# Optimization experiments

Measured on AMD Instinct MI355X. Metric: run time of the kernel, lower is better.

## Reference

```python
import jax, jax.numpy as jnp
import numpy as np

EMBED_DIM = 1024
N_HEADS = 16
KV_SIZE = 64
CLIP_DIST = 10
SLEN = 1024
BSZ = 8


def setup_inputs() -> dict:
    key = jax.random.key(0)
    ks = jax.random.split(key, 7)
    s = 0.02
    inputs = jax.random.normal(ks[0], (SLEN, BSZ, EMBED_DIM), dtype=jnp.float32)
    W_in = jax.random.normal(ks[1], (3 * N_HEADS * KV_SIZE, EMBED_DIM), dtype=jnp.float32) * s
    b_in = jnp.zeros((3 * N_HEADS * KV_SIZE,), dtype=jnp.float32)
    k_dist_emb = jax.random.normal(ks[2], (CLIP_DIST + 1, KV_SIZE), dtype=jnp.float32) * s
    v_dist_emb = jax.random.normal(ks[3], (CLIP_DIST + 1, KV_SIZE), dtype=jnp.float32) * s
    W_out = jax.random.normal(ks[4], (EMBED_DIM, N_HEADS * KV_SIZE), dtype=jnp.float32) * s
    b_out = jnp.zeros((EMBED_DIM,), dtype=jnp.float32)
    return {"inputs": inputs, "W_in": W_in, "b_in": b_in,
            "k_dist_emb": k_dist_emb, "v_dist_emb": v_dist_emb,
            "W_out": W_out, "b_out": b_out}


def reference(inputs, W_in, b_in, k_dist_emb, v_dist_emb, W_out, b_out):
    slen, bsz, _ = inputs.shape
    h, d = N_HEADS, KV_SIZE
    # in_proj: (slen, bsz, 3*h*d) -> (3, bsz, h, slen, d)
    qkv = inputs @ W_in.T + b_in
    qkv = qkv.reshape(slen, bsz, 3, h, d).transpose(2, 1, 3, 0, 4)
    q, k, v = qkv[0], qkv[1], qkv[2]
    q = q * (d ** -0.5)
    # clipped absolute relative distances (slen, slen)
    idx = jnp.arange(slen)
    dist = jnp.minimum(jnp.abs(idx[None, :] - idx[:, None]), CLIP_DIST)
    k_dist = k_dist_emb[dist]  # (slen, slen, d)
    v_dist = v_dist_emb[dist]  # (slen, slen, d)
    # content scores + relative-distance bias
    attn = jnp.einsum('bhsd,bhtd->bhst', q, k) + jnp.einsum('bhsd,std->bhst', q, k_dist)
    attn = jax.nn.softmax(attn, axis=-1)
    # value accumulation + relative-distance value correction
    out = jnp.einsum('bhst,bhtd->bhsd', attn, v) + jnp.einsum('bhst,std->bhsd', attn, v_dist)
    # (bsz, h, slen, d) -> (slen, bsz, h*d)
    out = out.transpose(2, 0, 1, 3).reshape(slen, bsz, h * d)
    return out @ W_out.T + b_out
```

## Files before the change

### kernel.cpp

```cpp
#include <hip/hip_runtime.h>
#include <hip/hip_bf16.h>
#include <cstdint>


typedef __attribute__((ext_vector_type(8))) __bf16 bf16x8;
typedef __attribute__((ext_vector_type(4))) __bf16 bf16x4;
typedef __attribute__((ext_vector_type(4))) short s16x4;
typedef __attribute__((ext_vector_type(4))) float f32x4;

#if __has_builtin(__builtin_amdgcn_exp2f)
#define EXP2F(x) __builtin_amdgcn_exp2f(x)
#else
#define EXP2F(x) exp2f(x)
#endif

#if __has_builtin(__builtin_amdgcn_mfma_f32_16x16x16bf16_1k)
#define PV_MFMA(ACC, AV, BV) \
  ACC = __builtin_amdgcn_mfma_f32_16x16x16bf16_1k( \
      __builtin_bit_cast(s16x4, AV), __builtin_bit_cast(s16x4, BV), ACC, 0, 0, 0)
#elif __has_builtin(__builtin_amdgcn_mfma_f32_16x16x16_bf16)
#define PV_MFMA(ACC, AV, BV) \
  ACC = __builtin_amdgcn_mfma_f32_16x16x16_bf16(AV, BV, ACC, 0, 0, 0)
#else
#define PV_MFMA(ACC, AV, BV)                                               \
  asm volatile("s_nop 1\n\tv_mfma_f32_16x16x16_bf16 %0, %1, %2, %0\n\t"    \
               "s_nop 7\n\ts_nop 7"                                        \
               : "+v"(ACC)                                                 \
               : "v"(__builtin_bit_cast(s16x4, AV)),                       \
                 "v"(__builtin_bit_cast(s16x4, BV)))
#endif

__device__ __forceinline__ void gload_lds16(const void* g, void* l) {
  __builtin_amdgcn_global_load_lds(
      (const __attribute__((address_space(1))) void*)g,
      (__attribute__((address_space(3))) void*)l, 16, 0, 0);
}

__global__ __launch_bounds__(256) void f2b3_kernel(
    const float* __restrict__ s0, __bf16* __restrict__ d0,
    const float* __restrict__ s1, __bf16* __restrict__ d1,
    const float* __restrict__ s2, __bf16* __restrict__ d2) {
  int i = (blockIdx.x * 256 + threadIdx.x) * 8;
  const float* s; __bf16* d; int off;
  if (i < 8388608) { s = s0; d = d0; off = i; }
  else if (i < 11534336) { s = s1; d = d1; off = i - 8388608; }
  else { s = s2; d = d2; off = i - 11534336; }
  float4 a = *(const float4*)(s + off);
  float4 b = *(const float4*)(s + off + 4);
  bf16x8 o;
  o[0] = (__bf16)a.x; o[1] = (__bf16)a.y; o[2] = (__bf16)a.z; o[3] = (__bf16)a.w;
  o[4] = (__bf16)b.x; o[5] = (__bf16)b.y; o[6] = (__bf16)b.z; o[7] = (__bf16)b.w;
  *(bf16x8*)(d + off) = o;
}


#define STG8A(SL, TK, G)                                                      \
  gload_lds16(A + (size_t)(m0 + (G) * 64 + (tid >> 3)) * K + (TK) * 64 + sgc, \
              (void*)&sG[SL][(G) * 4096 + wave * 512]);
#define STG8B(SL, TK, G)                                                      \
  gload_lds16(Bp + (size_t)(n0 + (G) * 64 + (tid >> 3)) * K + (TK) * 64 + sgc,\
              (void*)&sG[SL][16384 + (G) * 4096 + wave * 512]);

#define GPH(SL, MP, NP, STAGE_STMT, TAIL_STMT)                                  \
  {                                                                             \
    bf16x8 af[2][2], bfr[2][2];                                                 \
    _Pragma("unroll") for (int mi = 0; mi < 2; ++mi)                            \
      _Pragma("unroll") for (int kk = 0; kk < 2; ++kk)                          \
        af[mi][kk] = *(const bf16x8*)&sG[SL][                                   \
            (wr * 64 + ((MP) * 2 + mi) * 16 + lr) * 64 +                        \
            (((kk * 4 + lg) ^ (lr & 7)) * 8)];                                  \
    _Pragma("unroll") for (int ni = 0; ni < 2; ++ni)                            \
      _Pragma("unroll") for (int kk = 0; kk < 2; ++kk)                          \
        bfr[ni][kk] = *(const bf16x8*)&sG[SL][16384 +                           \
            (wc * 64 + ((NP) * 2 + ni) * 16 + lr) * 64 +                        \
            (((kk * 4 + lg) ^ (lr & 7)) * 8)];                                  \
    STAGE_STMT                                                                  \
    __builtin_amdgcn_s_barrier();                                               \
    asm volatile("s_waitcnt lgkmcnt(0)" ::: "memory");                          \
    __builtin_amdgcn_sched_barrier(0);                                          \
    __builtin_amdgcn_s_setprio(1);                                              \
    _Pragma("unroll") for (int mi = 0; mi < 2; ++mi)                            \
      _Pragma("unroll") for (int ni = 0; ni < 2; ++ni)                          \
        _Pragma("unroll") for (int kk = 0; kk < 2; ++kk)                        \
          acc[(MP) * 2 + mi][(NP) * 2 + ni] =                                   \
              __builtin_amdgcn_mfma_f32_16x16x32_bf16(                          \
                  af[mi][kk], bfr[ni][kk],                                      \
                  acc[(MP) * 2 + mi][(NP) * 2 + ni], 0, 0, 0);                  \
    __builtin_amdgcn_s_setprio(0);                                              \
    TAIL_STMT                                                                   \
    __builtin_amdgcn_s_barrier();                                               \
  }

#define GTILE(SL, SS, TK2, DOSTG, WAITC)                                        \
  GPH(SL, 0, 0, if (DOSTG) { STG8A(SS, TK2, 0) STG8A(SS, TK2, 1) }, )           \
  GPH(SL, 0, 1, if (DOSTG) { STG8A(SS, TK2, 2) STG8A(SS, TK2, 3) }, )           \
  GPH(SL, 1, 0, if (DOSTG) { STG8B(SS, TK2, 0) }, )                             \
  GPH(SL, 1, 1, if (DOSTG) { STG8B(SS, TK2, 1) },                               \
      if ((WAITC) == 6) { asm volatile("s_waitcnt vmcnt(6)" ::: "memory"); }    \
      else if ((WAITC) == 0) { asm volatile("s_waitcnt vmcnt(0)" ::: "memory"); })

template <int EPI>
__global__ __launch_bounds__(512) void gemm8p(
    const __bf16* __restrict__ A, const __bf16* __restrict__ Bp,
    const float* __restrict__ bias, int K,
    float* __restrict__ outF, __bf16* __restrict__ outT, int N, int NT, int CPX) {
  __shared__ __align__(16) __bf16 sG[3][24576];
  const int tid = threadIdx.x;
  const int wave = tid >> 6, lane = tid & 63;
  const int lg = lane >> 4, lr = lane & 15;
  const int wr = wave >> 1, wc = wave & 1;
  const int lid = (blockIdx.x & 7) * CPX + (blockIdx.x >> 3);
  const int m0 = (lid / NT) * 256;
  const int n0 = (lid % NT) * 128;

  const int sgc = ((tid & 7) ^ ((tid >> 3) & 7)) * 8;

  f32x4 acc[4][4] = {};

  STG8A(0, 0, 0) STG8A(0, 0, 1) STG8A(0, 0, 2) STG8A(0, 0, 3)
  STG8B(0, 0, 0) STG8B(0, 0, 1)
  STG8A(1, 1, 0) STG8A(1, 1, 1) STG8A(1, 1, 2) STG8A(1, 1, 3)
  STG8B(1, 1, 0) STG8B(1, 1, 1)
  asm volatile("s_waitcnt vmcnt(6)" ::: "memory");
  __builtin_amdgcn_s_barrier();

  GTILE(0, 2, 2, 1, 6)
  GTILE(1, 0, 3, 1, 6)
  GTILE(2, 1, 4, 1, 6)
  GTILE(0, 2, 5, 1, 6)
  GTILE(1, 0, 6, 1, 6)
  GTILE(2, 1, 7, 1, 6)
  GTILE(0, 2, 8, 1, 6)
  GTILE(1, 0, 9, 1, 6)
  GTILE(2, 1, 10, 1, 6)
  GTILE(0, 2, 11, 1, 6)
  GTILE(1, 0, 12, 1, 6)
  GTILE(2, 1, 13, 1, 6)
  GTILE(0, 2, 14, 1, 6)
  GTILE(1, 0, 15, 1, 6)
  GTILE(2, 1, 16, 0, 0)
  GTILE(0, 2, 17, 0, 2)

#pragma unroll
  for (int mf = 0; mf < 4; ++mf) {
    const int gm0 = m0 + wr * 64 + mf * 16 + lg * 4;
#pragma unroll
    for (int nf = 0; nf < 4; ++nf) {
      const int gn = n0 + wc * 64 + nf * 16 + lr;
      const float bv = bias[gn];
#pragma unroll
      for (int rg = 0; rg < 4; ++rg) {
        const int gm = gm0 + rg;
        float v = acc[mf][nf][rg] + bv;
        if constexpr (EPI == 0) {
          int t = gn >> 10, h = (gn >> 6) & 15, d = gn & 63;
          int s = gm >> 3, b = gm & 7;
          if (t == 0) v *= 0.18033688011112042f;
          outT[(((size_t)((t * 8 + b) * 16 + h) * 1024 + s) << 6) + d] = (__bf16)v;
        } else {
          outF[(size_t)gm * N + gn] = v;
        }
      }
    }
  }
}

__global__ __launch_bounds__(256) void vtrans_kernel(const __bf16* __restrict__ v,
                                                     __bf16* __restrict__ vt) {
  __shared__ __bf16 tile[64][66];
  const int tid = threadIdx.x;
  const int bh = blockIdx.x >> 4;
  const int s0 = (blockIdx.x & 15) * 64;
  const __bf16* src = v + ((size_t)bh * 1024 + s0) * 64;
#pragma unroll
  for (int it = 0; it < 4; ++it) {
    int idx = it * 256 + tid;
    int r = idx >> 4, c4 = (idx & 15) * 4;
    bf16x4 x = *(const bf16x4*)&src[r * 64 + c4];
    tile[r][c4 + 0] = x[0]; tile[r][c4 + 1] = x[1];
    tile[r][c4 + 2] = x[2]; tile[r][c4 + 3] = x[3];
  }
  __syncthreads();
  __bf16* dst = vt + (size_t)bh * 65536;
#pragma unroll
  for (int it = 0; it < 4; ++it) {
    int idx = it * 256 + tid;
    int dr = idx >> 4, s4 = (idx & 15) * 4;
    bf16x4 y;
    y[0] = tile[s4 + 0][dr]; y[1] = tile[s4 + 1][dr];
    y[2] = tile[s4 + 2][dr]; y[3] = tile[s4 + 3][dr];
    *(bf16x4*)&dst[(size_t)dr * 1024 + s0 + s4] = y;
  }
}

#define ATTN_TILE(KT, KC, KS, VC, VS)                                           \
  {                                                                             \
    if ((KT) < 15)                                                              \
      gload_lds16(vtp + (size_t)srow * 1024 + ((KT) + 1) * 64 + sc8,            \
                  &sV[VS][wave * 512]);                                         \
    if ((KT) < 14)                                                              \
      gload_lds16(kp + (size_t)((KT) * 64 + 128 + srow) * 64 + sc8,             \
                  &sK[KS][wave * 512]);                                         \
    f32x4 sf[4];                                                                \
    __builtin_amdgcn_s_setprio(1);                                              \
    _Pragma("unroll") for (int tj = 0; tj < 4; ++tj) {                          \
      const int t = tj * 16 + lr;                                               \
      bf16x8 bk0 = *(const bf16x8*)&sK[KC][t * 64 + ((lg ^ (t & 7)) * 8)];      \
      bf16x8 bk1 = *(const bf16x8*)&sK[KC][t * 64 + (((4 + lg) ^ (t & 7)) * 8)];\
      f32x4 z = {};                                                             \
      z = __builtin_amdgcn_mfma_f32_16x16x32_bf16(bk0, aq[0], z, 0, 0, 0);      \
      z = __builtin_amdgcn_mfma_f32_16x16x32_bf16(bk1, aq[1], z, 0, 0, 0);      \
      sf[tj] = z;                                                               \
    }                                                                           \
    __builtin_amdgcn_s_setprio(0);                                              \
    const bool inband = ((KT) * 64 <= sb + 24) && ((KT) * 64 + 63 >= sb - 9);   \
    if (inband) {                                                               \
      const float* bDrow = &sBD[wave][lr][0];                                   \
      _Pragma("unroll") for (int tj = 0; tj < 4; ++tj) {                        \
        _Pragma("unroll") for (int rg = 0; rg < 4; ++rg) {                      \
          const int t = (KT) * 64 + tj * 16 + lg * 4 + rg;                      \
          const int dd = t - s;                                                 \
          const int ad = dd < 0 ? -dd : dd;                                     \
          if (ad <= 9) {                                                        \
            const float val = sf[tj][rg] + bDrow[ad];                           \
            sf[tj][rg] = val;                                                   \
            band[wave][lr][dd + 9] = (__bf16)val;                               \
          }                                                                     \
        }                                                                       \
      }                                                                         \
    }                                                                           \
    float vm[4];                                                                \
    _Pragma("unroll") for (int tj = 0; tj < 4; ++tj)                            \
      vm[tj] = fmaxf(fmaxf(sf[tj][0], sf[tj][1]), fmaxf(sf[tj][2], sf[tj][3])); \
    float vmax = fmaxf(fmaxf(vm[0], vm[1]), fmaxf(vm[2], vm[3]));               \
    vmax = fmaxf(vmax, __shfl_xor(vmax, 16, 64));                               \
    vmax = fmaxf(vmax, __shfl_xor(vmax, 32, 64));                               \
    if (__any(vmax > m + 8.f)) {                                                \
      const float mn = fmaxf(m, vmax);                                          \
      const float scl = EXP2F(m - mn);                                          \
      m = mn;                                                                   \
      l *= scl;                                                                 \
      _Pragma("unroll") for (int dj = 0; dj < 4; ++dj)                          \
        _Pragma("unroll") for (int rg = 0; rg < 4; ++rg)                        \
          o_acc[dj][rg] *= scl;                                                 \
    }                                                                           \
    float rs[4];                                                                \
    _Pragma("unroll") for (int tj = 0; tj < 4; ++tj) {                          \
      float p0 = EXP2F(sf[tj][0] - m), p1 = EXP2F(sf[tj][1] - m);               \
      float p2 = EXP2F(sf[tj][2] - m), p3 = EXP2F(sf[tj][3] - m);               \
      sf[tj][0] = p0; sf[tj][1] = p1; sf[tj][2] = p2; sf[tj][3] = p3;           \
      rs[tj] = (p0 + p1) + (p2 + p3);                                           \
    }                                                                           \
    float rsum = (rs[0] + rs[1]) + (rs[2] + rs[3]);                             \
    rsum += __shfl_xor(rsum, 16, 64);                                           \
    rsum += __shfl_xor(rsum, 32, 64);                                           \
    l += rsum;                                                                  \
    bf16x4 pbv[4];                                                              \
    _Pragma("unroll") for (int tj = 0; tj < 4; ++tj) {                          \
      pbv[tj][0] = (__bf16)sf[tj][0]; pbv[tj][1] = (__bf16)sf[tj][1];           \
      pbv[tj][2] = (__bf16)sf[tj][2]; pbv[tj][3] = (__bf16)sf[tj][3];           \
    }                                                                           \
    __builtin_amdgcn_s_setprio(1);                                              \
    _Pragma("unroll") for (int tj = 0; tj < 4; ++tj) {                          \
      _Pragma("unroll") for (int dj = 0; dj < 4; ++dj) {                        \
        const int d = dj * 16 + lr;                                             \
        const int ch = (2 * tj + (lg >> 1)) ^ (d & 7);                          \
        const bf16x4 av = *(const bf16x4*)&sV[VC][d * 64 + ch * 8 + (lg & 1) * 4]; \
        PV_MFMA(o_acc[dj], av, pbv[tj]);                                        \
      }                                                                         \
    }                                                                           \
    __builtin_amdgcn_s_setprio(0);                                              \
    if ((KT) < 14) {                                                            \
      asm volatile("s_waitcnt vmcnt(1)" ::: "memory");                          \
    } else if ((KT) == 14) {                                                    \
      asm volatile("s_waitcnt vmcnt(0)" ::: "memory");                          \
    }                                                                           \
    if ((KT) < 15) __builtin_amdgcn_s_barrier();                                \
  }

__global__ __launch_bounds__(512) void attn_kernel(
    const __bf16* __restrict__ qkv, const __bf16* __restrict__ vt,
    const float* __restrict__ kde, const float* __restrict__ vde,
    __bf16* __restrict__ O) {
  __shared__ __align__(16) __bf16 sK[3][4096];
  __shared__ __align__(16) __bf16 sV[2][4096];
  __shared__ __bf16 band[8][16][20];
  __shared__ float sBD[8][16][10];
  const int tid = threadIdx.x, wave = tid >> 6, lane = tid & 63;
  const int lg = lane >> 4, lr = lane & 15;
  const int lid = (blockIdx.x & 7) * 128 + (blockIdx.x >> 3);
  const int bh = lid >> 3;
  const int stile = lid & 7;
  const int sb = stile * 128 + wave * 16;
  const int b = bh >> 4, h = bh & 15;
  const __bf16* qp = qkv + (size_t)bh * 65536;
  const __bf16* kp = qkv + (size_t)(128 + bh) * 65536;
  const __bf16* vtp = vt + (size_t)bh * 65536;

  const int srow = tid >> 3;
  const int sc8 = ((tid & 7) ^ (srow & 7)) * 8;

  gload_lds16(kp + (size_t)srow * 64 + sc8, &sK[0][wave * 512]);
  gload_lds16(vtp + (size_t)srow * 1024 + sc8, &sV[0][wave * 512]);
  gload_lds16(kp + (size_t)(64 + srow) * 64 + sc8, &sK[1][wave * 512]);

  {
    __bf16* bf = &band[0][0][0];
    for (int i = tid; i < 8 * 16 * 20; i += 512) bf[i] = (__bf16)(-1e30f);
  }

  bf16x8 aq[2];
#pragma unroll
  for (int kk = 0; kk < 2; ++kk)
    aq[kk] = *(const bf16x8*)&qp[(size_t)(sb + lr) * 64 + kk * 32 + lg * 8];

  {
    float kd10[16];
#pragma unroll
    for (int e = 0; e < 16; ++e)
      kd10[e] = kde[640 + (e >> 3) * 32 + lg * 8 + (e & 7)];
#pragma unroll
    for (int c = 0; c < 10; ++c) {
      float acc = 0.f;
#pragma unroll
      for (int e = 0; e < 16; ++e)
        acc += (float)aq[e >> 3][e & 7] *
               (kde[c * 64 + (e >> 3) * 32 + lg * 8 + (e & 7)] - kd10[e]);
      acc += __shfl_xor(acc, 16, 64);
      acc += __shfl_xor(acc, 32, 64);
      if (lg == 0) sBD[wave][lr][c] = acc;
    }
  }

  f32x4 o_acc[4] = {};
  float m = -1e30f, l = 0.f;
  const int s = sb + lr;

  asm volatile("s_waitcnt vmcnt(1)" ::: "memory");
  __builtin_amdgcn_s_barrier();

  ATTN_TILE( 0, 0, 2, 0, 1)
  ATTN_TILE( 1, 1, 0, 1, 0)
  ATTN_TILE( 2, 2, 1, 0, 1)
  ATTN_TILE( 3, 0, 2, 1, 0)
  ATTN_TILE( 4, 1, 0, 0, 1)
  ATTN_TILE( 5, 2, 1, 1, 0)
  ATTN_TILE( 6, 0, 2, 0, 1)
  ATTN_TILE( 7, 1, 0, 1, 0)
  ATTN_TILE( 8, 2, 1, 0, 1)
  ATTN_TILE( 9, 0, 2, 1, 0)
  ATTN_TILE(10, 1, 0, 0, 1)
  ATTN_TILE(11, 2, 1, 1, 0)
  ATTN_TILE(12, 0, 2, 0, 1)
  ATTN_TILE(13, 1, 0, 1, 0)
  ATTN_TILE(14, 2, 1, 0, 1)
  ATTN_TILE(15, 0, 2, 1, 0)

  const float inv = 1.f / l;
  float psum[10];
  psum[0] = EXP2F((float)band[wave][lr][9] - m);
#pragma unroll
  for (int c = 1; c < 10; ++c)
    psum[c] = EXP2F((float)band[wave][lr][9 - c] - m) +
              EXP2F((float)band[wave][lr][9 + c] - m);
#pragma unroll
  for (int dj = 0; dj < 4; ++dj) {
    bf16x4 ov;
#pragma unroll
    for (int rg = 0; rg < 4; ++rg) {
      const int d = dj * 16 + lg * 4 + rg;
      float acc2 = 0.f;
#pragma unroll
      for (int c = 0; c < 10; ++c)
        acc2 += psum[c] * (vde[c * 64 + d] - vde[640 + d]);
      ov[rg] = (__bf16)((o_acc[dj][rg] + acc2) * inv + vde[640 + d]);
    }
    *(bf16x4*)&O[((size_t)(s * 8 + b)) * 1024 + h * 64 + dj * 16 + lg * 4] = ov;
  }
}

extern "C" void kernel_launch(void* const* d_in, const int* in_sizes, int n_in,
                              void* d_out, int out_size, void* d_ws, size_t ws_size,
                              hipStream_t stream) {
  (void)in_sizes; (void)n_in; (void)out_size; (void)ws_size;
  const float* inputs = (const float*)d_in[0];
  const float* W_in   = (const float*)d_in[1];
  const float* b_in   = (const float*)d_in[2];
  const float* kde    = (const float*)d_in[3];
  const float* vde    = (const float*)d_in[4];
  const float* W_out  = (const float*)d_in[5];
  const float* b_out  = (const float*)d_in[6];
  float* out = (float*)d_out;

  char* ws = (char*)d_ws;
  __bf16* qkvt  = (__bf16*)(ws);
  __bf16* vt    = (__bf16*)(ws + 50331648);
  __bf16* Xb    = (__bf16*)(ws + 75497472);
  __bf16* Ob    = (__bf16*)(ws + 75497472);
  __bf16* Wb_in = (__bf16*)(ws + 92274688);
  __bf16* Wb_out= (__bf16*)(ws + 98566144);

  f2b3_kernel<<<6144, 256, 0, stream>>>(inputs, Xb, W_in, Wb_in, W_out, Wb_out);

  gemm8p<0><<<768, 512, 0, stream>>>(Xb, Wb_in, b_in, 1024, nullptr, qkvt, 3072, 24, 96);
  vtrans_kernel<<<2048, 256, 0, stream>>>(qkvt + (size_t)2 * 128 * 65536, vt);
  attn_kernel<<<1024, 512, 0, stream>>>(qkvt, vt, kde, vde, Ob);
  gemm8p<1><<<256, 512, 0, stream>>>(Ob, Wb_out, b_out, 1024, out, nullptr, 1024, 8, 32);
}
```

Baseline: 197.6 us.

## Fuse V transpose into QKV projection GEMM epilogue via LDS staging

The separate V-transpose kernel is removed. V-tiles of the input projection GEMM are now written transposed (d-major, s contiguous) directly from the epilogue, staged through shared memory so the global stores are 16-byte vectorised. This saves one kernel launch and a full read and write of the V tensor. The cost is extra LDS traffic and a barrier in one third of the GEMM blocks, and possible LDS bank conflicts in the scattered staging writes.

```diff
diff --git a/kernel.cpp b/kernel.cpp
--- a/kernel.cpp
+++ b/kernel.cpp
@@ -103,7 +103,8 @@
 __global__ __launch_bounds__(512) void gemm8p(
     const __bf16* __restrict__ A, const __bf16* __restrict__ Bp,
     const float* __restrict__ bias, int K,
-    float* __restrict__ outF, __bf16* __restrict__ outT, int N, int NT, int CPX) {
+    float* __restrict__ outF, __bf16* __restrict__ outT,
+    __bf16* __restrict__ outV, int N, int NT, int CPX) {
   __shared__ __align__(16) __bf16 sG[3][24576];
   const int tid = threadIdx.x;
   const int wave = tid >> 6, lane = tid & 63;
@@ -141,6 +142,43 @@
   GTILE(2, 1, 16, 0, 0)
   GTILE(0, 2, 17, 0, 2)
 
+  if constexpr (EPI == 0) {
+    const int tt = n0 >> 10;
+    if (tt == 2) {
+      __bf16* vtl = &sG[0][0];
+#pragma unroll
+      for (int mf = 0; mf < 4; ++mf) {
+#pragma unroll
+        for (int nf = 0; nf < 4; ++nf) {
+          const int gn = n0 + wc * 64 + nf * 16 + lr;
+          const float bv = bias[gn];
+          const int d = nf * 16 + lr;
+#pragma unroll
+          for (int rg = 0; rg < 4; ++rg) {
+            const int row = wr * 64 + mf * 16 + lg * 4 + rg;
+            const float v = acc[mf][nf][rg] + bv;
+            vtl[((size_t)((wc * 8 + (row & 7)) * 64 + d) << 5) + (row >> 3)] =
+                (__bf16)v;
+          }
+        }
+      }
+      __syncthreads();
+      const int s0g = m0 >> 3;
+      const int hh = (n0 >> 6) & 15;
+#pragma unroll
+      for (int rr = 0; rr < 2; ++rr) {
+        const int r = tid + rr * 512;
+        const int hl = r >> 9, bb = (r >> 6) & 7, dd = r & 63;
+        __bf16* dst = outV + ((size_t)((bb * 16 + hh + hl) * 64 + dd) << 10) + s0g;
+        const __bf16* src = &vtl[(size_t)r << 5];
+#pragma unroll
+        for (int j = 0; j < 4; ++j)
+          *(bf16x8*)&dst[j * 8] = *(const bf16x8*)&src[j * 8];
+      }
+      return;
+    }
+  }
+
 #pragma unroll
   for (int mf = 0; mf < 4; ++mf) {
     const int gm0 = m0 + wr * 64 + mf * 16 + lg * 4;
@@ -162,34 +200,6 @@
         }
       }
     }
-  }
-}
-
-__global__ __launch_bounds__(256) void vtrans_kernel(const __bf16* __restrict__ v,
-                                                     __bf16* __restrict__ vt) {
-  __shared__ __bf16 tile[64][66];
-  const int tid = threadIdx.x;
-  const int bh = blockIdx.x >> 4;
-  const int s0 = (blockIdx.x & 15) * 64;
-  const __bf16* src = v + ((size_t)bh * 1024 + s0) * 64;
-#pragma unroll
-  for (int it = 0; it < 4; ++it) {
-    int idx = it * 256 + tid;
-    int r = idx >> 4, c4 = (idx & 15) * 4;
-    bf16x4 x = *(const bf16x4*)&src[r * 64 + c4];
-    tile[r][c4 + 0] = x[0]; tile[r][c4 + 1] = x[1];
-    tile[r][c4 + 2] = x[2]; tile[r][c4 + 3] = x[3];
-  }
-  __syncthreads();
-  __bf16* dst = vt + (size_t)bh * 65536;
-#pragma unroll
-  for (int it = 0; it < 4; ++it) {
-    int idx = it * 256 + tid;
-    int dr = idx >> 4, s4 = (idx & 15) * 4;
-    bf16x4 y;
-    y[0] = tile[s4 + 0][dr]; y[1] = tile[s4 + 1][dr];
-    y[2] = tile[s4 + 2][dr]; y[3] = tile[s4 + 3][dr];
-    *(bf16x4*)&dst[(size_t)dr * 1024 + s0 + s4] = y;
   }
 }
 
@@ -402,8 +412,7 @@
 
   f2b3_kernel<<<6144, 256, 0, stream>>>(inputs, Xb, W_in, Wb_in, W_out, Wb_out);
 
-  gemm8p<0><<<768, 512, 0, stream>>>(Xb, Wb_in, b_in, 1024, nullptr, qkvt, 3072, 24, 96);
-  vtrans_kernel<<<2048, 256, 0, stream>>>(qkvt + (size_t)2 * 128 * 65536, vt);
+  gemm8p<0><<<768, 512, 0, stream>>>(Xb, Wb_in, b_in, 1024, nullptr, qkvt, vt, 3072, 24, 96);
   attn_kernel<<<1024, 512, 0, stream>>>(qkvt, vt, kde, vde, Ob);
-  gemm8p<1><<<256, 512, 0, stream>>>(Ob, Wb_out, b_out, 1024, out, nullptr, 1024, 8, 32);
+  gemm8p<1><<<256, 512, 0, stream>>>(Ob, Wb_out, b_out, 1024, out, nullptr, nullptr, 1024, 8, 32);
 }
```

Measured after the change: 195.4 us, median of 2. No clear change (-1.1%).
